# Optimization experiments

Measured on AMD Instinct MI355X. Metric: run time of the kernel, lower is better.

The kernel has to match this reference:

```python
import jax, jax.numpy as jnp
import numpy as np

EPS = 1e-6          # VN leaky-relu denominator eps (vn_layers.py)
NEG_SLOPE = 0.2     # VNLinearLeakyReLU default negative_slope
K = 3               # pointops.interpolation default k
DIST_EPS = 1e-8     # interpolation inverse-distance eps


def vn_linear_leakyrelu(x, w_feat, w_dir):
    # x: [B, Cin, 3, N]; w_*: [Cout, Cin]  (bias-free Linears over channel dim)
    p = jnp.einsum('oc,bcvn->bovn', w_feat, x)
    d = jnp.einsum('oc,bcvn->bovn', w_dir, x)
    dot = jnp.sum(p * d, axis=2, keepdims=True)          # [B,Cout,1,N]
    d2 = jnp.sum(d * d, axis=2, keepdims=True)
    mask = (dot >= 0).astype(x.dtype)
    proj = p - (dot / (d2 + EPS)) * d                    # reflect negative part onto plane perp to d
    return NEG_SLOPE * p + (1.0 - NEG_SLOPE) * (mask * p + (1.0 - mask) * proj)


def interpolation(p2, p1, feat, b, n2, n1):
    # p2: [b*n2,3] coarse coords, p1: [b*n1,3] fine coords, feat: [C,3,b*n2]
    # k-NN inverse-squared-distance interpolation, segment-local per cloud.
    C = feat.shape[0]
    p2b = p2.reshape(b, n2, 3)
    p1b = p1.reshape(b, n1, 3)
    featb = feat.reshape(C * 3, b, n2).transpose(1, 2, 0)  # [b, n2, C*3]

    def per_batch(q, s, f):
        d2 = jnp.sum((q[:, None, :] - s[None, :, :]) ** 2, axis=-1)  # [n1,n2]
        neg_d2, idx = jax.lax.top_k(-d2, K)                          # k smallest sq-dists
        w = 1.0 / (-neg_d2 + DIST_EPS)
        w = w / jnp.sum(w, axis=1, keepdims=True)                    # [n1,K]
        return jnp.einsum('nk,nkc->nc', w, f[idx])                   # [n1, C*3]

    out = jax.vmap(per_batch)(p1b, p2b, featb)                       # [b, n1, C*3]
    return out.reshape(b, n1, C, 3).transpose(2, 3, 0, 1).reshape(C, 3, b * n1)


def setup_inputs() -> dict:
    key = jax.random.key(0)
    ks = jax.random.split(key, 8)
    b, n1, n2 = 4, 16384, 4096
    in_planes, out_planes = 128, 64
    p1 = jax.random.uniform(ks[0], (b * n1, 3), dtype=jnp.float32)
    p2 = jax.random.uniform(ks[1], (b * n2, 3), dtype=jnp.float32)
    x1 = jax.random.normal(ks[2], (1, out_planes, 3, b * n1), dtype=jnp.float32)
    x2 = jax.random.normal(ks[3], (1, in_planes, 3, b * n2), dtype=jnp.float32)
    o1 = (jnp.arange(1, b + 1, dtype=jnp.int32)) * n1   # cumulative offsets
    o2 = (jnp.arange(1, b + 1, dtype=jnp.int32)) * n2
    s1 = 1.0 / np.sqrt(out_planes)
    s2 = 1.0 / np.sqrt(in_planes)
    w1_feat = jax.random.uniform(ks[4], (out_planes, out_planes), jnp.float32, -s1, s1)
    w1_dir = jax.random.uniform(ks[5], (out_planes, out_planes), jnp.float32, -s1, s1)
    w2_feat = jax.random.uniform(ks[6], (out_planes, in_planes), jnp.float32, -s2, s2)
    w2_dir = jax.random.uniform(ks[7], (out_planes, in_planes), jnp.float32, -s2, s2)
    return {"p1": p1, "x1": x1, "o1": o1, "p2": p2, "x2": x2, "o2": o2,
            "w1_feat": w1_feat, "w1_dir": w1_dir, "w2_feat": w2_feat, "w2_dir": w2_dir}


def reference(p1, x1, o1, p2, x2, o2, w1_feat, w1_dir, w2_feat, w2_dir):
    b = o1.shape[0]
    n1 = x1.shape[-1] // b
    n2 = x2.shape[-1] // b
    y1 = vn_linear_leakyrelu(x1, w1_feat, w1_dir)            # [1,Cout,3,N1]
    y2 = vn_linear_leakyrelu(x2, w2_feat, w2_dir)[0]         # squeeze(0) -> [Cout,3,N2]
    up = interpolation(p2, p1, y2, b, n2, n1)                # [Cout,3,N1]
    return y1 + up
```

## Files before the change

kernel.cpp:

```cpp
#include <hip/hip_runtime.h>

#define N1T 65536
#define N2T 16384
#define COUT 64
#define CH 192
#define GRD 8
#define HCELL 0.125f

typedef unsigned short bhalf;
typedef __attribute__((ext_vector_type(8))) short short8;
typedef __attribute__((ext_vector_type(4))) float f32x4;

__device__ __forceinline__ bhalf f2bf(float f) {
    unsigned u = __float_as_uint(f);
    return (bhalf)((u + 0x7FFFu + ((u >> 16) & 1u)) >> 16);
}
__device__ __forceinline__ float bf2f(bhalf h) {
    return __uint_as_float(((unsigned)h) << 16);
}

__global__ __launch_bounds__(256) void wconv_kernel(
    const float* __restrict__ w1f, const float* __restrict__ w1d,
    const float* __restrict__ w2f, const float* __restrict__ w2d,
    bhalf* __restrict__ o1fh, bhalf* __restrict__ o1fl,
    bhalf* __restrict__ o1dh, bhalf* __restrict__ o1dl,
    bhalf* __restrict__ o2fh, bhalf* __restrict__ o2fl,
    bhalf* __restrict__ o2dh, bhalf* __restrict__ o2dl) {
    const int i = blockIdx.x * 256 + threadIdx.x;
    if (i < 4096) {
        const float a = w1f[i]; const bhalf ah = f2bf(a);
        o1fh[i] = ah; o1fl[i] = f2bf(a - bf2f(ah));
        const float b = w1d[i]; const bhalf bh = f2bf(b);
        o1dh[i] = bh; o1dl[i] = f2bf(b - bf2f(bh));
    }
    const float a = w2f[i]; const bhalf ah = f2bf(a);
    o2fh[i] = ah; o2fl[i] = f2bf(a - bf2f(ah));
    const float b = w2d[i]; const bhalf bh = f2bf(b);
    o2dh[i] = bh; o2dl[i] = f2bf(b - bf2f(bh));
}

template<int CIN, int N, bool CM, int NT>
__global__ __launch_bounds__(512) void vn_mfma_kernel(
    const float* __restrict__ x,
    const bhalf* __restrict__ wfh, const bhalf* __restrict__ wfl,
    const bhalf* __restrict__ wdh, const bhalf* __restrict__ wdl,
    const int*   __restrict__ idxs,
    const float* __restrict__ wts,
    const float* __restrict__ y2t,
    float* __restrict__ out)
{
    constexpr int ROWS = CIN * 3;
    constexpr int LDSC = CIN * 3 + 8;
    constexpr int NB   = (NT > 1) ? 2 : 1;
    constexpr int NLD  = ROWS * 8 / 512;
    __shared__ __align__(16) bhalf xs_h[NB][32][LDSC];
    __shared__ __align__(16) bhalf xs_l[NB][32][LDSC];

    const int tid  = threadIdx.x;
    const int lane = tid & 63;
    const int wave = tid >> 6;
    const int r16  = lane & 15;
    const int hh   = lane >> 4;
    const int ot   = wave & 3;
    const int sW   = wave >> 2;
    const int pt   = sW * 16 + r16;
    const int tile0 = blockIdx.x * NT;

    int gk[NT][3]; float gw[NT][3];
    if constexpr (CM) {
#pragma unroll
        for (int t = 0; t < NT; ++t) {
            const int n = (tile0 + t) * 32 + pt;
#pragma unroll
            for (int r = 0; r < 3; ++r) {
                gk[t][r] = idxs[r * N1T + n];
                gw[t][r] = wts[r * N1T + n];
            }
        }
    }

    const int wofs = (ot * 16 + r16) * CIN + hh * 8;
    const bhalf* __restrict__ pfh = wfh + wofs;
    const bhalf* __restrict__ pfl = wfl + wofs;
    const bhalf* __restrict__ pdh = wdh + wofs;
    const bhalf* __restrict__ pdl = wdl + wofs;
    const int hs = ((hh ^ (r16 >> 2)) & 3) * 8;

    auto LOADT = [&](float4 (&st)[NLD], int t) {
#pragma unroll
        for (int r = 0; r < NLD; ++r) {
            const int i4 = r * 512 + tid;
            const int row = i4 >> 3, p4 = i4 & 7;
            st[r] = *(const float4*)&x[(size_t)row * N + (size_t)(tile0 + t) * 32 + p4 * 4];
        }
    };
    auto WRITET = [&](const float4 (&st)[NLD], int b) {
#pragma unroll
        for (int r = 0; r < NLD; ++r) {
            const int i4 = r * 512 + tid;
            const int row = i4 >> 3, p4 = i4 & 7;
            const int c = row / 3, vv = row - c * 3;
            const int colS = (vv * CIN + c) ^ ((p4 & 3) << 3);
            const float vals[4] = {st[r].x, st[r].y, st[r].z, st[r].w};
#pragma unroll
            for (int j = 0; j < 4; ++j) {
                const bhalf h = f2bf(vals[j]);
                xs_h[b][p4*4+j][colS] = h;
                xs_l[b][p4*4+j][colS] = f2bf(vals[j] - bf2f(h));
            }
        }
    };
    auto COMPUTET = [&](int t, int b, const int (&gkt)[3], const float (&gwt)[3]) {
        const f32x4 zero = {0.f, 0.f, 0.f, 0.f};
        f32x4 accP[3], accD[3];
#pragma unroll
        for (int v = 0; v < 3; ++v) { accP[v] = zero; accD[v] = zero; }
#pragma unroll
        for (int k = 0; k < CIN / 32; ++k) {
            const short8 afh = *(const short8*)(pfh + k * 32);
            const short8 afl = *(const short8*)(pfl + k * 32);
            const short8 adh = *(const short8*)(pdh + k * 32);
            const short8 adl = *(const short8*)(pdl + k * 32);
#pragma unroll
            for (int v = 0; v < 3; ++v) {
                const short8 bh = *(const short8*)&xs_h[b][pt][v * CIN + k * 32 + hs];
                const short8 bl = *(const short8*)&xs_l[b][pt][v * CIN + k * 32 + hs];
                accP[v] = __builtin_amdgcn_mfma_f32_16x16x32_bf16(afh, bh, accP[v], 0, 0, 0);
                accP[v] = __builtin_amdgcn_mfma_f32_16x16x32_bf16(afl, bh, accP[v], 0, 0, 0);
                accP[v] = __builtin_amdgcn_mfma_f32_16x16x32_bf16(afh, bl, accP[v], 0, 0, 0);
                accD[v] = __builtin_amdgcn_mfma_f32_16x16x32_bf16(adh, bh, accD[v], 0, 0, 0);
                accD[v] = __builtin_amdgcn_mfma_f32_16x16x32_bf16(adl, bh, accD[v], 0, 0, 0);
                accD[v] = __builtin_amdgcn_mfma_f32_16x16x32_bf16(adh, bl, accD[v], 0, 0, 0);
            }
        }
        float rr[12];
#pragma unroll
        for (int reg = 0; reg < 4; ++reg) {
            const float p0 = accP[0][reg], p1 = accP[1][reg], p2 = accP[2][reg];
            const float q0 = accD[0][reg], q1 = accD[1][reg], q2 = accD[2][reg];
            const float dot = p0*q0 + p1*q1 + p2*q2;
            const float dd  = q0*q0 + q1*q1 + q2*q2;
            const float coef = (dot < 0.f) ? (0.8f * dot / (dd + 1e-6f)) : 0.f;
            rr[reg*3+0] = p0 - coef * q0;
            rr[reg*3+1] = p1 - coef * q1;
            rr[reg*3+2] = p2 - coef * q2;
        }
        const int n = (tile0 + t) * 32 + pt;
        if constexpr (!CM) {
            float* op = out + (size_t)n * CH + ot * 48 + hh * 12;
            *(float4*)&op[0] = make_float4(rr[0], rr[1], rr[2],  rr[3]);
            *(float4*)&op[4] = make_float4(rr[4], rr[5], rr[6],  rr[7]);
            *(float4*)&op[8] = make_float4(rr[8], rr[9], rr[10], rr[11]);
        } else {
            const int chb = ot * 48 + hh * 12;
            const float* __restrict__ r0 = y2t + (size_t)gkt[0] * CH + chb;
            const float* __restrict__ r1 = y2t + (size_t)gkt[1] * CH + chb;
            const float* __restrict__ r2 = y2t + (size_t)gkt[2] * CH + chb;
            const float w0 = gwt[0], w1 = gwt[1], w2 = gwt[2];
            float4 a0[3], a1[3], a2[3];
#pragma unroll
            for (int q = 0; q < 3; ++q) {
                a0[q] = *(const float4*)&r0[q * 4];
                a1[q] = *(const float4*)&r1[q * 4];
                a2[q] = *(const float4*)&r2[q * 4];
            }
#pragma unroll
            for (int q = 0; q < 3; ++q) {
                const float u0 = w0*a0[q].x + w1*a1[q].x + w2*a2[q].x;
                const float u1 = w0*a0[q].y + w1*a1[q].y + w2*a2[q].y;
                const float u2 = w0*a0[q].z + w1*a1[q].z + w2*a2[q].z;
                const float u3 = w0*a0[q].w + w1*a1[q].w + w2*a2[q].w;
                out[(size_t)(chb + q*4 + 0) * N + n] = rr[q*4+0] + u0;
                out[(size_t)(chb + q*4 + 1) * N + n] = rr[q*4+1] + u1;
                out[(size_t)(chb + q*4 + 2) * N + n] = rr[q*4+2] + u2;
                out[(size_t)(chb + q*4 + 3) * N + n] = rr[q*4+3] + u3;
            }
        }
    };

    float4 stA[NLD], stB[NLD];
    LOADT(stA, 0);
    WRITET(stA, 0);
    if constexpr (NT == 2) {
        LOADT(stB, 1);
        __syncthreads();
        COMPUTET(0, 0, gk[0], gw[0]);
        WRITET(stB, 1);
        __syncthreads();
        COMPUTET(1, 1, gk[1], gw[1]);
    } else {
        __syncthreads();
        COMPUTET(0, 0, gk[0], gw[0]);
    }
}

#define KNN_INSERT(d2, j)                                        \
    {                                                            \
        const bool c0 = (d2) < b0;                               \
        const bool c1 = (d2) < b1;                               \
        const bool c2 = (d2) < b2v;                              \
        const float nb2 = c2 ? (c1 ? b1 : (d2)) : b2v;           \
        const int   ni2 = c2 ? (c1 ? i1 : (j))  : i2;            \
        const float nb1 = c1 ? (c0 ? b0 : (d2)) : b1;            \
        const int   ni1 = c1 ? (c0 ? i0 : (j))  : i1;            \
        b0 = c0 ? (d2) : b0;  i0 = c0 ? (j) : i0;                \
        b1 = nb1; i1 = ni1; b2v = nb2; i2 = ni2;                 \
    }

__global__ __launch_bounds__(256) void zero_kernel(int* __restrict__ p, int n) {
    const int i = blockIdx.x * 256 + threadIdx.x;
    if (i < n) p[i] = 0;
}

__device__ __forceinline__ int cell_of(float x, float y, float z) {
    int cx = (int)(x * (float)GRD); cx = cx < 0 ? 0 : (cx > GRD-1 ? GRD-1 : cx);
    int cy = (int)(y * (float)GRD); cy = cy < 0 ? 0 : (cy > GRD-1 ? GRD-1 : cy);
    int cz = (int)(z * (float)GRD); cz = cz < 0 ? 0 : (cz > GRD-1 ? GRD-1 : cz);
    return (cz << 6) | (cy << 3) | cx;
}

__global__ __launch_bounds__(256) void bin_count_kernel(
    const float* __restrict__ p2, int* __restrict__ counts) {
    const int i = blockIdx.x * 256 + threadIdx.x;
    const float x = p2[i*3+0], y = p2[i*3+1], z = p2[i*3+2];
    const int cell = ((i >> 12) << 9) | cell_of(x, y, z);
    atomicAdd(&counts[cell], 1);
}

__global__ __launch_bounds__(256) void scan_kernel(
    const int* __restrict__ counts, int* __restrict__ off) {
    __shared__ int buf[2][256];
    const int t = threadIdx.x;
    int v[8]; int s = 0;
#pragma unroll
    for (int j = 0; j < 8; ++j) { const int tmp = counts[t*8+j]; v[j] = s; s += tmp; }
    buf[0][t] = s; __syncthreads();
    int src = 0;
    for (int d = 1; d < 256; d <<= 1) {
        int val = buf[src][t];
        if (t >= d) val += buf[src][t - d];
        buf[src ^ 1][t] = val; src ^= 1; __syncthreads();
    }
    const int incl = buf[src][t];
    const int base = incl - s;
#pragma unroll
    for (int j = 0; j < 8; ++j) off[t*8+j] = base + v[j];
    if (t == 255) off[2048] = incl;
}

__global__ __launch_bounds__(256) void bin_scatter_kernel(
    const float* __restrict__ p2, const int* __restrict__ off,
    int* __restrict__ cnt2, float4* __restrict__ binned) {
    const int i = blockIdx.x * 256 + threadIdx.x;
    const float x = p2[i*3+0], y = p2[i*3+1], z = p2[i*3+2];
    const int cell = ((i >> 12) << 9) | cell_of(x, y, z);
    const int pos = off[cell] + atomicAdd(&cnt2[cell], 1);
    binned[pos] = make_float4(x, y, z, __int_as_float(i));
}

__global__ __launch_bounds__(256) void knn_grid_kernel(
    const float* __restrict__ p1,
    const float4* __restrict__ binned,
    const int* __restrict__ off,
    int*   __restrict__ idx_out,
    float* __restrict__ w_out)
{
    const int t   = blockIdx.x * 256 + threadIdx.x;
    const int fp  = t >> 2;
    const int sub = t & 3;
    const int bi  = fp >> 14;
    const int cbase = bi << 9;

    const float qx = p1[fp*3+0], qy = p1[fp*3+1], qz = p1[fp*3+2];
    int cx = (int)(qx * (float)GRD); cx = cx < 0 ? 0 : (cx > 7 ? 7 : cx);
    int cy = (int)(qy * (float)GRD); cy = cy < 0 ? 0 : (cy > 7 ? 7 : cy);
    int cz = (int)(qz * (float)GRD); cz = cz < 0 ? 0 : (cz > 7 ? 7 : cz);

    const int x0 = cx > 0 ? cx - 1 : 0;
    const int x1 = cx < 7 ? cx + 1 : 7;

    float b0 = 1e30f, b1 = 1e30f, b2v = 1e30f;
    int   i0 = 0,     i1 = 0,     i2 = 0;

#pragma unroll
    for (int dz = -1; dz <= 1; ++dz) {
        const int nz = cz + dz;
        if ((unsigned)nz > 7u) continue;
#pragma unroll
        for (int dy = -1; dy <= 1; ++dy) {
            const int ny = cy + dy;
            if ((unsigned)ny > 7u) continue;
            const int cb = cbase + (nz << 6) + (ny << 3);
            const int s = off[cb + x0], e = off[cb + x1 + 1];
            for (int k = s + sub; k < e; k += 4) {
                const float4 c4 = binned[k];
                const float ddx = qx - c4.x, ddy = qy - c4.y, ddz = qz - c4.z;
                const float d2 = fmaf(ddx, ddx, fmaf(ddy, ddy, ddz * ddz));
                const int j = __float_as_int(c4.w);
                KNN_INSERT(d2, j)
            }
        }
    }

#pragma unroll
    for (int m = 1; m <= 2; m <<= 1) {
        const float c0v = __shfl_xor(b0, m, 4);
        const float c1v = __shfl_xor(b1, m, 4);
        const float c2v = __shfl_xor(b2v, m, 4);
        const int   j0v = __shfl_xor(i0, m, 4);
        const int   j1v = __shfl_xor(i1, m, 4);
        const int   j2v = __shfl_xor(i2, m, 4);
        KNN_INSERT(c0v, j0v)
        KNN_INSERT(c1v, j1v)
        KNN_INSERT(c2v, j2v)
    }

    float dw = 1e30f;
    if (cx >= 2) dw = fminf(dw, qx - (float)(cx - 1) * HCELL);
    if (cx <= 5) dw = fminf(dw, (float)(cx + 2) * HCELL - qx);
    if (cy >= 2) dw = fminf(dw, qy - (float)(cy - 1) * HCELL);
    if (cy <= 5) dw = fminf(dw, (float)(cy + 2) * HCELL - qy);
    if (cz >= 2) dw = fminf(dw, qz - (float)(cz - 1) * HCELL);
    if (cz <= 5) dw = fminf(dw, (float)(cz + 2) * HCELL - qz);
    const bool done = b2v < dw * dw;

    if (!done) {
        b0 = b1 = b2v = 1e30f; i0 = i1 = i2 = 0;
        const int s = bi << 12, e = (bi + 1) << 12;
        for (int k = s + sub; k < e; k += 4) {
            const float4 c4 = binned[k];
            const float ddx = qx - c4.x, ddy = qy - c4.y, ddz = qz - c4.z;
            const float d2 = fmaf(ddx, ddx, fmaf(ddy, ddy, ddz * ddz));
            const int j = __float_as_int(c4.w);
            KNN_INSERT(d2, j)
        }
#pragma unroll
        for (int m = 1; m <= 2; m <<= 1) {
            const float c0v = __shfl_xor(b0, m, 4);
            const float c1v = __shfl_xor(b1, m, 4);
            const float c2v = __shfl_xor(b2v, m, 4);
            const int   j0v = __shfl_xor(i0, m, 4);
            const int   j1v = __shfl_xor(i1, m, 4);
            const int   j2v = __shfl_xor(i2, m, 4);
            KNN_INSERT(c0v, j0v)
            KNN_INSERT(c1v, j1v)
            KNN_INSERT(c2v, j2v)
        }
    }

    if (sub == 0) {
        const float w0 = 1.f / (b0 + 1e-8f);
        const float w1 = 1.f / (b1 + 1e-8f);
        const float w2 = 1.f / (b2v + 1e-8f);
        const float inv = 1.f / (w0 + w1 + w2);
        idx_out[0*N1T + fp] = i0;
        idx_out[1*N1T + fp] = i1;
        idx_out[2*N1T + fp] = i2;
        w_out[0*N1T + fp] = w0 * inv;
        w_out[1*N1T + fp] = w1 * inv;
        w_out[2*N1T + fp] = w2 * inv;
    }
}

extern "C" void kernel_launch(void* const* d_in, const int* in_sizes, int n_in,
                              void* d_out, int out_size, void* d_ws, size_t ws_size,
                              hipStream_t stream) {
    const float* p1      = (const float*)d_in[0];
    const float* x1      = (const float*)d_in[1];
    const float* p2      = (const float*)d_in[3];
    const float* x2      = (const float*)d_in[4];
    const float* w1_feat = (const float*)d_in[6];
    const float* w1_dir  = (const float*)d_in[7];
    const float* w2_feat = (const float*)d_in[8];
    const float* w2_dir  = (const float*)d_in[9];
    float* out = (float*)d_out;

    char* ws = (char*)d_ws;
    float*  y2t    = (float*)ws;                 ws += (size_t)N2T * CH * 4;
    int*    idxs   = (int*)ws;                   ws += (size_t)3 * N1T * 4;
    float*  wts    = (float*)ws;                 ws += (size_t)3 * N1T * 4;
    int*    counts = (int*)ws;                   ws += 2048 * 4;
    int*    cnt2   = (int*)ws;                   ws += 2048 * 4;
    int*    off    = (int*)ws;                   ws += 2064 * 4;
    float4* binned = (float4*)ws;                ws += (size_t)N2T * 16;
    bhalf*  wb1fh  = (bhalf*)ws;                 ws += 4096 * 2;
    bhalf*  wb1fl  = (bhalf*)ws;                 ws += 4096 * 2;
    bhalf*  wb1dh  = (bhalf*)ws;                 ws += 4096 * 2;
    bhalf*  wb1dl  = (bhalf*)ws;                 ws += 4096 * 2;
    bhalf*  wb2fh  = (bhalf*)ws;                 ws += 8192 * 2;
    bhalf*  wb2fl  = (bhalf*)ws;                 ws += 8192 * 2;
    bhalf*  wb2dh  = (bhalf*)ws;                 ws += 8192 * 2;
    bhalf*  wb2dl  = (bhalf*)ws;                 ws += 8192 * 2;

    wconv_kernel<<<32, 256, 0, stream>>>(w1_feat, w1_dir, w2_feat, w2_dir,
                                         wb1fh, wb1fl, wb1dh, wb1dl,
                                         wb2fh, wb2fl, wb2dh, wb2dl);

    zero_kernel<<<16, 256, 0, stream>>>(counts, 4096);
    bin_count_kernel<<<N2T/256, 256, 0, stream>>>(p2, counts);
    scan_kernel<<<1, 256, 0, stream>>>(counts, off);
    bin_scatter_kernel<<<N2T/256, 256, 0, stream>>>(p2, off, cnt2, binned);
    knn_grid_kernel<<<(4*N1T)/256, 256, 0, stream>>>(p1, binned, off, idxs, wts);

    vn_mfma_kernel<128, N2T, false, 1><<<N2T/32, 512, 0, stream>>>(
        x2, wb2fh, wb2fl, wb2dh, wb2dl, nullptr, nullptr, nullptr, y2t);
    vn_mfma_kernel<64, N1T, true, 2><<<N1T/64, 512, 0, stream>>>(
        x1, wb1fh, wb1fl, wb1dh, wb1dl, idxs, wts, y2t, out);
}
```

Before: 98.50 us.

## Fuse coarse VN layer with kNN search into one role-split kernel; merge zeroing into prep

The coarse-level VN linear/leaky-ReLU (MFMA bf16x3) and the grid kNN search now run in a single launch, with even blocks computing y2 and odd blocks doing kNN for 128 query points. Weight conversion and count zeroing are merged into one prep kernel. This removes two launches and lets the two independent workloads run side by side on the GPU. The cost is that kNN blocks now use 512 threads and carry the VN kernel's LDS allocation, which may lower occupancy for the kNN part.

```diff
diff --git a/kernel.cpp b/kernel.cpp
--- a/kernel.cpp
+++ b/kernel.cpp
@@ -19,24 +19,30 @@
     return __uint_as_float(((unsigned)h) << 16);
 }
 
-__global__ __launch_bounds__(256) void wconv_kernel(
+__global__ __launch_bounds__(256) void prep_kernel(
     const float* __restrict__ w1f, const float* __restrict__ w1d,
     const float* __restrict__ w2f, const float* __restrict__ w2d,
     bhalf* __restrict__ o1fh, bhalf* __restrict__ o1fl,
     bhalf* __restrict__ o1dh, bhalf* __restrict__ o1dl,
     bhalf* __restrict__ o2fh, bhalf* __restrict__ o2fl,
-    bhalf* __restrict__ o2dh, bhalf* __restrict__ o2dl) {
-    const int i = blockIdx.x * 256 + threadIdx.x;
-    if (i < 4096) {
-        const float a = w1f[i]; const bhalf ah = f2bf(a);
-        o1fh[i] = ah; o1fl[i] = f2bf(a - bf2f(ah));
-        const float b = w1d[i]; const bhalf bh = f2bf(b);
-        o1dh[i] = bh; o1dl[i] = f2bf(b - bf2f(bh));
-    }
-    const float a = w2f[i]; const bhalf ah = f2bf(a);
-    o2fh[i] = ah; o2fl[i] = f2bf(a - bf2f(ah));
-    const float b = w2d[i]; const bhalf bh = f2bf(b);
-    o2dh[i] = bh; o2dl[i] = f2bf(b - bf2f(bh));
+    bhalf* __restrict__ o2dh, bhalf* __restrict__ o2dl,
+    int* __restrict__ zp) {
+    if (blockIdx.x < 32) {
+        const int i = blockIdx.x * 256 + threadIdx.x;
+        if (i < 4096) {
+            const float a = w1f[i]; const bhalf ah = f2bf(a);
+            o1fh[i] = ah; o1fl[i] = f2bf(a - bf2f(ah));
+            const float b = w1d[i]; const bhalf bh = f2bf(b);
+            o1dh[i] = bh; o1dl[i] = f2bf(b - bf2f(bh));
+        }
+        const float a = w2f[i]; const bhalf ah = f2bf(a);
+        o2fh[i] = ah; o2fl[i] = f2bf(a - bf2f(ah));
+        const float b = w2d[i]; const bhalf bh = f2bf(b);
+        o2dh[i] = bh; o2dl[i] = f2bf(b - bf2f(bh));
+    } else {
+        const int i = (blockIdx.x - 32) * 256 + threadIdx.x;
+        if (i < 4096) zp[i] = 0;
+    }
 }
 
 template<int CIN, int N, bool CM, int NT>
@@ -207,11 +213,6 @@
         b1 = nb1; i1 = ni1; b2v = nb2; i2 = ni2;                 \
     }
 
-__global__ __launch_bounds__(256) void zero_kernel(int* __restrict__ p, int n) {
-    const int i = blockIdx.x * 256 + threadIdx.x;
-    if (i < n) p[i] = 0;
-}
-
 __device__ __forceinline__ int cell_of(float x, float y, float z) {
     int cx = (int)(x * (float)GRD); cx = cx < 0 ? 0 : (cx > GRD-1 ? GRD-1 : cx);
     int cy = (int)(y * (float)GRD); cy = cy < 0 ? 0 : (cy > GRD-1 ? GRD-1 : cy);
@@ -258,82 +259,137 @@
     binned[pos] = make_float4(x, y, z, __int_as_float(i));
 }
 
-__global__ __launch_bounds__(256) void knn_grid_kernel(
+__global__ __launch_bounds__(512) void vn2_knn_kernel(
+    const float* __restrict__ x2,
+    const bhalf* __restrict__ wfh, const bhalf* __restrict__ wfl,
+    const bhalf* __restrict__ wdh, const bhalf* __restrict__ wdl,
+    float* __restrict__ y2t,
     const float* __restrict__ p1,
     const float4* __restrict__ binned,
     const int* __restrict__ off,
     int*   __restrict__ idx_out,
     float* __restrict__ w_out)
 {
-    const int t   = blockIdx.x * 256 + threadIdx.x;
-    const int fp  = t >> 2;
-    const int sub = t & 3;
-    const int bi  = fp >> 14;
-    const int cbase = bi << 9;
-
-    const float qx = p1[fp*3+0], qy = p1[fp*3+1], qz = p1[fp*3+2];
-    int cx = (int)(qx * (float)GRD); cx = cx < 0 ? 0 : (cx > 7 ? 7 : cx);
-    int cy = (int)(qy * (float)GRD); cy = cy < 0 ? 0 : (cy > 7 ? 7 : cy);
-    int cz = (int)(qz * (float)GRD); cz = cz < 0 ? 0 : (cz > 7 ? 7 : cz);
-
-    const int x0 = cx > 0 ? cx - 1 : 0;
-    const int x1 = cx < 7 ? cx + 1 : 7;
-
-    float b0 = 1e30f, b1 = 1e30f, b2v = 1e30f;
-    int   i0 = 0,     i1 = 0,     i2 = 0;
-
-#pragma unroll
-    for (int dz = -1; dz <= 1; ++dz) {
-        const int nz = cz + dz;
-        if ((unsigned)nz > 7u) continue;
-#pragma unroll
-        for (int dy = -1; dy <= 1; ++dy) {
-            const int ny = cy + dy;
-            if ((unsigned)ny > 7u) continue;
-            const int cb = cbase + (nz << 6) + (ny << 3);
-            const int s = off[cb + x0], e = off[cb + x1 + 1];
-            for (int k = s + sub; k < e; k += 4) {
-                const float4 c4 = binned[k];
-                const float ddx = qx - c4.x, ddy = qy - c4.y, ddz = qz - c4.z;
-                const float d2 = fmaf(ddx, ddx, fmaf(ddy, ddy, ddz * ddz));
-                const int j = __float_as_int(c4.w);
-                KNN_INSERT(d2, j)
-            }
-        }
-    }
-
-#pragma unroll
-    for (int m = 1; m <= 2; m <<= 1) {
-        const float c0v = __shfl_xor(b0, m, 4);
-        const float c1v = __shfl_xor(b1, m, 4);
-        const float c2v = __shfl_xor(b2v, m, 4);
-        const int   j0v = __shfl_xor(i0, m, 4);
-        const int   j1v = __shfl_xor(i1, m, 4);
-        const int   j2v = __shfl_xor(i2, m, 4);
-        KNN_INSERT(c0v, j0v)
-        KNN_INSERT(c1v, j1v)
-        KNN_INSERT(c2v, j2v)
-    }
-
-    float dw = 1e30f;
-    if (cx >= 2) dw = fminf(dw, qx - (float)(cx - 1) * HCELL);
-    if (cx <= 5) dw = fminf(dw, (float)(cx + 2) * HCELL - qx);
-    if (cy >= 2) dw = fminf(dw, qy - (float)(cy - 1) * HCELL);
-    if (cy <= 5) dw = fminf(dw, (float)(cy + 2) * HCELL - qy);
-    if (cz >= 2) dw = fminf(dw, qz - (float)(cz - 1) * HCELL);
-    if (cz <= 5) dw = fminf(dw, (float)(cz + 2) * HCELL - qz);
-    const bool done = b2v < dw * dw;
-
-    if (!done) {
-        b0 = b1 = b2v = 1e30f; i0 = i1 = i2 = 0;
-        const int s = bi << 12, e = (bi + 1) << 12;
-        for (int k = s + sub; k < e; k += 4) {
-            const float4 c4 = binned[k];
-            const float ddx = qx - c4.x, ddy = qy - c4.y, ddz = qz - c4.z;
-            const float d2 = fmaf(ddx, ddx, fmaf(ddy, ddy, ddz * ddz));
-            const int j = __float_as_int(c4.w);
-            KNN_INSERT(d2, j)
-        }
+    constexpr int CIN = 128, N = N2T;
+    constexpr int LDSC = CIN * 3 + 8;
+    __shared__ __align__(16) bhalf xs_h[32][LDSC];
+    __shared__ __align__(16) bhalf xs_l[32][LDSC];
+
+    const int role = blockIdx.x & 1;
+    const int ridx = blockIdx.x >> 1;
+    const int tid  = threadIdx.x;
+
+    if (role == 0) {
+        const int lane = tid & 63;
+        const int wave = tid >> 6;
+        const int r16  = lane & 15;
+        const int hh   = lane >> 4;
+        const int ot   = wave & 3;
+        const int sW   = wave >> 2;
+        const int pt   = sW * 16 + r16;
+        const int n0   = ridx * 32;
+
+        const int wofs = (ot * 16 + r16) * CIN + hh * 8;
+        const bhalf* __restrict__ pfh = wfh + wofs;
+        const bhalf* __restrict__ pfl = wfl + wofs;
+        const bhalf* __restrict__ pdh = wdh + wofs;
+        const bhalf* __restrict__ pdl = wdl + wofs;
+        const int hs = ((hh ^ (r16 >> 2)) & 3) * 8;
+
+#pragma unroll
+        for (int r = 0; r < 6; ++r) {
+            const int i4 = r * 512 + tid;
+            const int row = i4 >> 3, p4 = i4 & 7;
+            const float4 v = *(const float4*)&x2[(size_t)row * N + n0 + p4 * 4];
+            const int c = row / 3, vv = row - c * 3;
+            const int colS = (vv * CIN + c) ^ ((p4 & 3) << 3);
+            const float vals[4] = {v.x, v.y, v.z, v.w};
+#pragma unroll
+            for (int j = 0; j < 4; ++j) {
+                const bhalf h = f2bf(vals[j]);
+                xs_h[p4*4+j][colS] = h;
+                xs_l[p4*4+j][colS] = f2bf(vals[j] - bf2f(h));
+            }
+        }
+        __syncthreads();
+
+        const f32x4 zero = {0.f, 0.f, 0.f, 0.f};
+        f32x4 accP[3], accD[3];
+#pragma unroll
+        for (int v = 0; v < 3; ++v) { accP[v] = zero; accD[v] = zero; }
+#pragma unroll
+        for (int k = 0; k < CIN / 32; ++k) {
+            const short8 afh = *(const short8*)(pfh + k * 32);
+            const short8 afl = *(const short8*)(pfl + k * 32);
+            const short8 adh = *(const short8*)(pdh + k * 32);
+            const short8 adl = *(const short8*)(pdl + k * 32);
+#pragma unroll
+            for (int v = 0; v < 3; ++v) {
+                const short8 bh = *(const short8*)&xs_h[pt][v * CIN + k * 32 + hs];
+                const short8 bl = *(const short8*)&xs_l[pt][v * CIN + k * 32 + hs];
+                accP[v] = __builtin_amdgcn_mfma_f32_16x16x32_bf16(afh, bh, accP[v], 0, 0, 0);
+                accP[v] = __builtin_amdgcn_mfma_f32_16x16x32_bf16(afl, bh, accP[v], 0, 0, 0);
+                accP[v] = __builtin_amdgcn_mfma_f32_16x16x32_bf16(afh, bl, accP[v], 0, 0, 0);
+                accD[v] = __builtin_amdgcn_mfma_f32_16x16x32_bf16(adh, bh, accD[v], 0, 0, 0);
+                accD[v] = __builtin_amdgcn_mfma_f32_16x16x32_bf16(adl, bh, accD[v], 0, 0, 0);
+                accD[v] = __builtin_amdgcn_mfma_f32_16x16x32_bf16(adh, bl, accD[v], 0, 0, 0);
+            }
+        }
+
+        float rr[12];
+#pragma unroll
+        for (int reg = 0; reg < 4; ++reg) {
+            const float p0 = accP[0][reg], p1 = accP[1][reg], p2 = accP[2][reg];
+            const float q0 = accD[0][reg], q1 = accD[1][reg], q2 = accD[2][reg];
+            const float dot = p0*q0 + p1*q1 + p2*q2;
+            const float dd  = q0*q0 + q1*q1 + q2*q2;
+            const float coef = (dot < 0.f) ? (0.8f * dot / (dd + 1e-6f)) : 0.f;
+            rr[reg*3+0] = p0 - coef * q0;
+            rr[reg*3+1] = p1 - coef * q1;
+            rr[reg*3+2] = p2 - coef * q2;
+        }
+        const int n = n0 + pt;
+        float* op = y2t + (size_t)n * CH + ot * 48 + hh * 12;
+        *(float4*)&op[0] = make_float4(rr[0], rr[1], rr[2],  rr[3]);
+        *(float4*)&op[4] = make_float4(rr[4], rr[5], rr[6],  rr[7]);
+        *(float4*)&op[8] = make_float4(rr[8], rr[9], rr[10], rr[11]);
+    } else {
+        const int fp  = ridx * 128 + (tid >> 2);
+        const int sub = tid & 3;
+        const int bi  = fp >> 14;
+        const int cbase = bi << 9;
+
+        const float qx = p1[fp*3+0], qy = p1[fp*3+1], qz = p1[fp*3+2];
+        int cx = (int)(qx * (float)GRD); cx = cx < 0 ? 0 : (cx > 7 ? 7 : cx);
+        int cy = (int)(qy * (float)GRD); cy = cy < 0 ? 0 : (cy > 7 ? 7 : cy);
+        int cz = (int)(qz * (float)GRD); cz = cz < 0 ? 0 : (cz > 7 ? 7 : cz);
+
+        const int x0 = cx > 0 ? cx - 1 : 0;
+        const int x1 = cx < 7 ? cx + 1 : 7;
+
+        float b0 = 1e30f, b1 = 1e30f, b2v = 1e30f;
+        int   i0 = 0,     i1 = 0,     i2 = 0;
+
+#pragma unroll
+        for (int dz = -1; dz <= 1; ++dz) {
+            const int nz = cz + dz;
+            if ((unsigned)nz > 7u) continue;
+#pragma unroll
+            for (int dy = -1; dy <= 1; ++dy) {
+                const int ny = cy + dy;
+                if ((unsigned)ny > 7u) continue;
+                const int cb = cbase + (nz << 6) + (ny << 3);
+                const int s = off[cb + x0], e = off[cb + x1 + 1];
+                for (int k = s + sub; k < e; k += 4) {
+                    const float4 c4 = binned[k];
+                    const float ddx = qx - c4.x, ddy = qy - c4.y, ddz = qz - c4.z;
+                    const float d2 = fmaf(ddx, ddx, fmaf(ddy, ddy, ddz * ddz));
+                    const int j = __float_as_int(c4.w);
+                    KNN_INSERT(d2, j)
+                }
+            }
+        }
+
 #pragma unroll
         for (int m = 1; m <= 2; m <<= 1) {
             const float c0v = __shfl_xor(b0, m, 4);
@@ -346,19 +402,52 @@
             KNN_INSERT(c1v, j1v)
             KNN_INSERT(c2v, j2v)
         }
-    }
-
-    if (sub == 0) {
-        const float w0 = 1.f / (b0 + 1e-8f);
-        const float w1 = 1.f / (b1 + 1e-8f);
-        const float w2 = 1.f / (b2v + 1e-8f);
-        const float inv = 1.f / (w0 + w1 + w2);
-        idx_out[0*N1T + fp] = i0;
-        idx_out[1*N1T + fp] = i1;
-        idx_out[2*N1T + fp] = i2;
-        w_out[0*N1T + fp] = w0 * inv;
-        w_out[1*N1T + fp] = w1 * inv;
-        w_out[2*N1T + fp] = w2 * inv;
+
+        float dw = 1e30f;
+        if (cx >= 2) dw = fminf(dw, qx - (float)(cx - 1) * HCELL);
+        if (cx <= 5) dw = fminf(dw, (float)(cx + 2) * HCELL - qx);
+        if (cy >= 2) dw = fminf(dw, qy - (float)(cy - 1) * HCELL);
+        if (cy <= 5) dw = fminf(dw, (float)(cy + 2) * HCELL - qy);
+        if (cz >= 2) dw = fminf(dw, qz - (float)(cz - 1) * HCELL);
+        if (cz <= 5) dw = fminf(dw, (float)(cz + 2) * HCELL - qz);
+        const bool done = b2v < dw * dw;
+
+        if (!done) {
+            b0 = b1 = b2v = 1e30f; i0 = i1 = i2 = 0;
+            const int s = bi << 12, e = (bi + 1) << 12;
+            for (int k = s + sub; k < e; k += 4) {
+                const float4 c4 = binned[k];
+                const float ddx = qx - c4.x, ddy = qy - c4.y, ddz = qz - c4.z;
+                const float d2 = fmaf(ddx, ddx, fmaf(ddy, ddy, ddz * ddz));
+                const int j = __float_as_int(c4.w);
+                KNN_INSERT(d2, j)
+            }
+#pragma unroll
+            for (int m = 1; m <= 2; m <<= 1) {
+                const float c0v = __shfl_xor(b0, m, 4);
+                const float c1v = __shfl_xor(b1, m, 4);
+                const float c2v = __shfl_xor(b2v, m, 4);
+                const int   j0v = __shfl_xor(i0, m, 4);
+                const int   j1v = __shfl_xor(i1, m, 4);
+                const int   j2v = __shfl_xor(i2, m, 4);
+                KNN_INSERT(c0v, j0v)
+                KNN_INSERT(c1v, j1v)
+                KNN_INSERT(c2v, j2v)
+            }
+        }
+
+        if (sub == 0) {
+            const float w0 = 1.f / (b0 + 1e-8f);
+            const float w1 = 1.f / (b1 + 1e-8f);
+            const float w2 = 1.f / (b2v + 1e-8f);
+            const float inv = 1.f / (w0 + w1 + w2);
+            idx_out[0*N1T + fp] = i0;
+            idx_out[1*N1T + fp] = i1;
+            idx_out[2*N1T + fp] = i2;
+            w_out[0*N1T + fp] = w0 * inv;
+            w_out[1*N1T + fp] = w1 * inv;
+            w_out[2*N1T + fp] = w2 * inv;
+        }
     }
 }
 
@@ -392,18 +481,15 @@
     bhalf*  wb2dh  = (bhalf*)ws;                 ws += 8192 * 2;
     bhalf*  wb2dl  = (bhalf*)ws;                 ws += 8192 * 2;
 
-    wconv_kernel<<<32, 256, 0, stream>>>(w1_feat, w1_dir, w2_feat, w2_dir,
-                                         wb1fh, wb1fl, wb1dh, wb1dl,
-                                         wb2fh, wb2fl, wb2dh, wb2dl);
-
-    zero_kernel<<<16, 256, 0, stream>>>(counts, 4096);
+    prep_kernel<<<48, 256, 0, stream>>>(w1_feat, w1_dir, w2_feat, w2_dir,
+                                        wb1fh, wb1fl, wb1dh, wb1dl,
+                                        wb2fh, wb2fl, wb2dh, wb2dl, counts);
     bin_count_kernel<<<N2T/256, 256, 0, stream>>>(p2, counts);
     scan_kernel<<<1, 256, 0, stream>>>(counts, off);
     bin_scatter_kernel<<<N2T/256, 256, 0, stream>>>(p2, off, cnt2, binned);
-    knn_grid_kernel<<<(4*N1T)/256, 256, 0, stream>>>(p1, binned, off, idxs, wts);
-
-    vn_mfma_kernel<128, N2T, false, 1><<<N2T/32, 512, 0, stream>>>(
-        x2, wb2fh, wb2fl, wb2dh, wb2dl, nullptr, nullptr, nullptr, y2t);
+    vn2_knn_kernel<<<1024, 512, 0, stream>>>(
+        x2, wb2fh, wb2fl, wb2dh, wb2dl, y2t,
+        p1, binned, off, idxs, wts);
     vn_mfma_kernel<64, N1T, true, 2><<<N1T/64, 512, 0, stream>>>(
         x1, wb1fh, wb1fl, wb1dh, wb1dl, idxs, wts, y2t, out);
 }
```

Result: no change. 98.95 us (+0.5%).
